# Kernel tuning notes

Measured on AMD Instinct MI355X. Metric: run time of the kernel, lower is better.

## Reference

```python
import jax, jax.numpy as jnp
import numpy as np

B = 8192          # batch of sequences (original module used 1; math broadcasts)
T = 99            # sequential FastGRNN steps
D_IN = 32         # per-step input features (3168 = 99 * 32)
D_H = 100         # hidden size
R_W, R_U = 16, 25 # low ranks
N_CLS = 6


def setup_inputs() -> dict:
    key = jax.random.key(0)
    ks = jax.random.split(key, 11)
    s = 0.1
    return {
        "x": jax.random.normal(ks[0], (B, T * D_IN), dtype=jnp.float32),
        "W1": jax.random.normal(ks[1], (D_IN, R_W), dtype=jnp.float32) * s,
        "W2": jax.random.normal(ks[2], (R_W, D_H), dtype=jnp.float32) * s,
        "U1": jax.random.normal(ks[3], (D_H, R_U), dtype=jnp.float32) * s,
        "U2": jax.random.normal(ks[4], (R_U, D_H), dtype=jnp.float32) * s,
        "bias_gate": jax.random.normal(ks[5], (1, D_H), dtype=jnp.float32) * s,
        "bias_update": jax.random.normal(ks[6], (1, D_H), dtype=jnp.float32) * s,
        "zeta": jax.random.normal(ks[7], (1, 1), dtype=jnp.float32),
        "nu": jax.random.normal(ks[8], (1, 1), dtype=jnp.float32),
        "FC": jax.random.normal(ks[9], (D_H, N_CLS), dtype=jnp.float32) * s,
        "FCbias": jax.random.normal(ks[10], (1, N_CLS), dtype=jnp.float32) * s,
    }


def reference(x, W1, W2, U1, U2, bias_gate, bias_update, zeta, nu, FC, FCbias):
    b = x.shape[0]
    # x[:, 32*i:32*(i+1)] for i in 0..T-1  ->  [T, B, D_IN] for scan
    xs = x.reshape(b, T, D_IN).transpose(1, 0, 2)
    sz = jax.nn.sigmoid(zeta)  # [1,1]
    sn = jax.nn.sigmoid(nu)    # [1,1]
    H0 = jnp.zeros((b, D_H), dtype=x.dtype)

    def step(H, XX):
        # low-rank projections: (XX @ W1) @ W2 + (H @ U1) @ U2
        c = (XX @ W1) @ W2 + (H @ U1) @ U2          # [B, D_H]
        g = jax.nn.sigmoid(c + bias_gate)
        h = jnp.tanh(c + bias_update)
        # exact blend from source: tanh branch is NOT scaled by (1-g)
        H_new = g * H + (sz * (1.0 - g) + sn * h)
        return H_new, None

    H, _ = jax.lax.scan(step, H0, xs)
    score = H @ FC + FCbias                          # [B, N_CLS]
    return score
```

## Files before the change

kernel.cpp:

```cpp
#include <hip/hip_runtime.h>
#include <math.h>


typedef __attribute__((ext_vector_type(8))) short short8_t;
typedef __attribute__((ext_vector_type(4))) float f32x4;

#define TSTEPS 99
#define DIN    32
#define DH     100
#define XROW   3168
#define NCLS   6
#define LOG2E  1.44269504088896340736f

#define NFRAG  70
#define OFF_EG (NFRAG * 256)
#define OFF_EU (OFF_EG + 128)
#define OFF_SZ (OFF_EU + 128)
#define OFF_SN (OFF_SZ + 1)

__device__ __forceinline__ unsigned cvtpk(float a, float b) {
    unsigned r;
    asm("v_cvt_pk_bf16_f32 %0, %1, %2" : "=v"(r) : "v"(a), "v"(b));
    return r;
}
__device__ __forceinline__ float fbits(unsigned u) { return __int_as_float((int)u); }

union F8 { unsigned u4[4]; short8_t s8; };

__global__ __launch_bounds__(256) void precomp(
    const float* __restrict__ W1, const float* __restrict__ W2,
    const float* __restrict__ U1, const float* __restrict__ U2,
    const float* __restrict__ bg, const float* __restrict__ bu,
    const float* __restrict__ zeta, const float* __restrict__ nu,
    float* __restrict__ ws)
{
    const int i = blockIdx.x * 256 + threadIdx.x;
    if (i < 2240) {
        const int lane = i & 63, f = i >> 6;
        const int jt = f / 5, kt = f % 5;
        const int u = lane & 15, g4 = lane >> 4;
        const int col = jt * 16 + u;
        float v[8];
        #pragma unroll
        for (int e = 0; e < 8; ++e) {
            float s = 0.f;
            if (col < DH) {
                if (kt < 4) {
                    const int k = kt * 32 + g4 * 8 + e;
                    if (k < DH) {
                        #pragma unroll
                        for (int r = 0; r < 25; ++r)
                            s = fmaf(U1[k * 25 + r], U2[r * DH + col], s);
                    }
                } else {
                    const int k = g4 * 8 + e;
                    #pragma unroll
                    for (int r = 0; r < 16; ++r)
                        s = fmaf(W1[k * 16 + r], W2[r * DH + col], s);
                }
            }
            v[e] = s * LOG2E;
        }
        unsigned hi[4], lo[4];
        #pragma unroll
        for (int rr = 0; rr < 4; ++rr) {
            const float a = v[2 * rr], b = v[2 * rr + 1];
            const unsigned ph = cvtpk(a, b);
            hi[rr] = ph;
            lo[rr] = cvtpk(a - fbits(ph << 16), b - fbits(ph & 0xffff0000u));
        }
        uint4* B = (uint4*)ws;
        B[(f * 2 + 0) * 64 + lane] = make_uint4(hi[0], hi[1], hi[2], hi[3]);
        B[(f * 2 + 1) * 64 + lane] = make_uint4(lo[0], lo[1], lo[2], lo[3]);
    } else if (i < 2240 + 128) {
        const int p = i - 2240;
        ws[OFF_EG + p] = (p < DH) ? expf(-bg[p]) : 1.f;
    } else if (i < 2240 + 256) {
        const int p = i - 2240 - 128;
        ws[OFF_EU + p] = (p < DH) ? expf(-2.f * bu[p]) : 1.f;
    } else if (i == 2240 + 256) {
        ws[OFF_SZ] = 1.f / (1.f + expf(-zeta[0]));
    } else if (i == 2240 + 257) {
        ws[OFF_SN] = 1.f / (1.f + expf(-nu[0]));
    }
}

__global__ __launch_bounds__(256, 2) void fastgrnn_main(
    const float* __restrict__ x, const float* __restrict__ ws,
    const float* __restrict__ FC, const float* __restrict__ FCbias,
    float* __restrict__ out)
{
    __shared__ __align__(16) float Hl[2][16][132];

    const int tid  = threadIdx.x;
    const int lane = tid & 63;
    const int ww   = __builtin_amdgcn_readfirstlane(tid >> 6);
    const int jn   = (ww == 3) ? 1 : 2;
    const int u    = lane & 15;
    const int g4   = lane >> 4;
    const int rowbase = blockIdx.x * 16;

    for (int z = tid; z < 2 * 16 * 132; z += 256) ((float*)Hl)[z] = 0.f;

    F8 Breg[2][5][2];
    #pragma unroll
    for (int jj = 0; jj < 2; ++jj) {
        const int jt = (2 * ww + jj > 6) ? 6 : 2 * ww + jj;
        #pragma unroll
        for (int kt = 0; kt < 5; ++kt) {
            #pragma unroll
            for (int s = 0; s < 2; ++s) {
                const int F = (jt * 5 + kt) * 2 + s;
                Breg[jj][kt][s].s8 =
                    *(const short8_t*)((const uint4*)ws + F * 64 + lane);
                asm volatile("" : "+v"(Breg[jj][kt][s].u4[0]),
                                  "+v"(Breg[jj][kt][s].u4[1]),
                                  "+v"(Breg[jj][kt][s].u4[2]),
                                  "+v"(Breg[jj][kt][s].u4[3]));
            }
        }
    }
    float eg_r[2], eu_r[2];
    #pragma unroll
    for (int jj = 0; jj < 2; ++jj) {
        const int jt = (2 * ww + jj > 6) ? 6 : 2 * ww + jj;
        const int unit = jt * 16 + u;
        eg_r[jj] = ws[OFF_EG + unit];
        eu_r[jj] = ws[OFF_EU + unit];
        asm volatile("" : "+v"(eg_r[jj]), "+v"(eu_r[jj]));
    }
    const float sz = ws[OFF_SZ];
    const float sn = ws[OFF_SN];

    const float* __restrict__ xrow = x + (size_t)(rowbase + u) * XROW + g4 * 8;

    const f32x4 zero4 = {0.f, 0.f, 0.f, 0.f};
    f32x4 Hold[2];
    Hold[0] = zero4; Hold[1] = zero4;

    __syncthreads();

    for (int t = 0; t < TSTEPS; ++t) {
        const int rb = t & 1, wb = rb ^ 1;

        F8 xhi, xlo;
        {
            const f32x4 xa = *(const f32x4*)(xrow + t * DIN);
            const f32x4 xb = *(const f32x4*)(xrow + t * DIN + 4);
            const float xs[8] = { xa.x, xa.y, xa.z, xa.w, xb.x, xb.y, xb.z, xb.w };
            #pragma unroll
            for (int r = 0; r < 4; ++r) {
                const unsigned ph = cvtpk(xs[2*r], xs[2*r+1]);
                xhi.u4[r] = ph;
                xlo.u4[r] = cvtpk(xs[2*r]   - fbits(ph << 16),
                                  xs[2*r+1] - fbits(ph & 0xffff0000u));
            }
        }

        F8 ahi[4], alo[4];
        #pragma unroll
        for (int kt = 0; kt < 4; ++kt) {
            const f32x4 h0 = *(const f32x4*)&Hl[rb][u][kt * 32 + g4 * 8];
            const f32x4 h1 = *(const f32x4*)&Hl[rb][u][kt * 32 + g4 * 8 + 4];
            const float hs[8] = { h0.x, h0.y, h0.z, h0.w, h1.x, h1.y, h1.z, h1.w };
            #pragma unroll
            for (int r = 0; r < 4; ++r) {
                const unsigned ph = cvtpk(hs[2*r], hs[2*r+1]);
                ahi[kt].u4[r] = ph;
                alo[kt].u4[r] = cvtpk(hs[2*r]   - fbits(ph << 16),
                                      hs[2*r+1] - fbits(ph & 0xffff0000u));
            }
        }

        f32x4 acc[2];
        acc[0] = zero4; acc[1] = zero4;

        #pragma unroll
        for (int kt = 0; kt < 5; ++kt) {
            const short8_t Ah = (kt < 4) ? ahi[kt].s8 : xhi.s8;
            const short8_t Al = (kt < 4) ? alo[kt].s8 : xlo.s8;
            #pragma unroll
            for (int jj = 0; jj < 2; ++jj)
                if (jj < jn)
                    acc[jj] = __builtin_amdgcn_mfma_f32_16x16x32_bf16(
                        Al, Breg[jj][kt][0].s8, acc[jj], 0, 0, 0);
            #pragma unroll
            for (int jj = 0; jj < 2; ++jj)
                if (jj < jn)
                    acc[jj] = __builtin_amdgcn_mfma_f32_16x16x32_bf16(
                        Ah, Breg[jj][kt][1].s8, acc[jj], 0, 0, 0);
            #pragma unroll
            for (int jj = 0; jj < 2; ++jj)
                if (jj < jn)
                    acc[jj] = __builtin_amdgcn_mfma_f32_16x16x32_bf16(
                        Ah, Breg[jj][kt][0].s8, acc[jj], 0, 0, 0);
        }

        #pragma unroll
        for (int jj = 0; jj < 2; ++jj) {
            if (jj < jn) {
                f32x4 hn;
                #pragma unroll
                for (int i = 0; i < 4; ++i) {
                    const float cc = acc[jj][i];
                    const float E  = __builtin_amdgcn_exp2f(-cc);
                    const float g  = __builtin_amdgcn_rcpf(fmaf(E, eg_r[jj], 1.f));
                    float p = E * E * eu_r[jj];
                    p = fminf(p, 1e30f);
                    const float h = (1.f - p) * __builtin_amdgcn_rcpf(1.f + p);
                    hn[i] = fmaf(g, Hold[jj][i], fmaf(sn, h, fmaf(-sz, g, sz)));
                }
                Hold[jj] = hn;
                const int unit = (2 * ww + jj) * 16 + u;
                Hl[wb][g4 * 4 + 0][unit] = hn[0];
                Hl[wb][g4 * 4 + 1][unit] = hn[1];
                Hl[wb][g4 * 4 + 2][unit] = hn[2];
                Hl[wb][g4 * 4 + 3][unit] = hn[3];
            }
        }
        __syncthreads();
    }

    const int fb = TSTEPS & 1;
    if (tid < 16 * NCLS) {
        const int rl = tid / NCLS, c = tid % NCLS;
        float s = FCbias[c];
        for (int k = 0; k < DH; ++k)
            s = fmaf(Hl[fb][rl][k], FC[k * NCLS + c], s);
        out[(size_t)(rowbase + rl) * NCLS + c] = s;
    }
}

extern "C" void kernel_launch(void* const* d_in, const int* in_sizes, int n_in,
                              void* d_out, int out_size, void* d_ws, size_t ws_size,
                              hipStream_t stream)
{
    const float* x    = (const float*)d_in[0];
    const float* W1   = (const float*)d_in[1];
    const float* W2   = (const float*)d_in[2];
    const float* U1   = (const float*)d_in[3];
    const float* U2   = (const float*)d_in[4];
    const float* bg   = (const float*)d_in[5];
    const float* bu   = (const float*)d_in[6];
    const float* zeta = (const float*)d_in[7];
    const float* nu   = (const float*)d_in[8];
    const float* FC   = (const float*)d_in[9];
    const float* FCb  = (const float*)d_in[10];
    float* ws  = (float*)d_ws;
    float* out = (float*)d_out;

    precomp<<<(2240 + 258 + 255) / 256, 256, 0, stream>>>(
        W1, W2, U1, U2, bg, bu, zeta, nu, ws);
    fastgrnn_main<<<512, 256, 0, stream>>>(x, ws, FC, FCb, out);
}
```

Before: 311.1 us.

## Store hidden state as pre-split bf16 hi/lo pairs in swizzled LDS

```diff
diff --git a/kernel.cpp b/kernel.cpp
--- a/kernel.cpp
+++ b/kernel.cpp
@@ -90,7 +90,7 @@
     const float* __restrict__ FC, const float* __restrict__ FCbias,
     float* __restrict__ out)
 {
-    __shared__ __align__(16) float Hl[2][16][132];
+    __shared__ unsigned Hs[2][2][16][68];
 
     const int tid  = threadIdx.x;
     const int lane = tid & 63;
@@ -100,7 +100,7 @@
     const int g4   = lane >> 4;
     const int rowbase = blockIdx.x * 16;
 
-    for (int z = tid; z < 2 * 16 * 132; z += 256) ((float*)Hl)[z] = 0.f;
+    for (int z = tid; z < 2 * 2 * 16 * 68; z += 256) ((unsigned*)Hs)[z] = 0u;
 
     F8 Breg[2][5][2];
     #pragma unroll
@@ -138,6 +138,9 @@
     f32x4 Hold[2];
     Hold[0] = zero4; Hold[1] = zero4;
 
+    const int ridx0 = (g4 ^ (u & 3)) << 2;
+    unsigned short* const hwbase = (unsigned short*)&Hs[0][0][0][0];
+
     __syncthreads();
 
     for (int t = 0; t < TSTEPS; ++t) {
@@ -157,28 +160,14 @@
             }
         }
 
-        F8 ahi[4], alo[4];
+        f32x4 a0[2], a1[2];
+        a0[0] = zero4; a0[1] = zero4; a1[0] = zero4; a1[1] = zero4;
+
         #pragma unroll
         for (int kt = 0; kt < 4; ++kt) {
-            const f32x4 h0 = *(const f32x4*)&Hl[rb][u][kt * 32 + g4 * 8];
-            const f32x4 h1 = *(const f32x4*)&Hl[rb][u][kt * 32 + g4 * 8 + 4];
-            const float hs[8] = { h0.x, h0.y, h0.z, h0.w, h1.x, h1.y, h1.z, h1.w };
-            #pragma unroll
-            for (int r = 0; r < 4; ++r) {
-                const unsigned ph = cvtpk(hs[2*r], hs[2*r+1]);
-                ahi[kt].u4[r] = ph;
-                alo[kt].u4[r] = cvtpk(hs[2*r]   - fbits(ph << 16),
-                                      hs[2*r+1] - fbits(ph & 0xffff0000u));
-            }
-        }
-
-        f32x4 acc[2];
-        acc[0] = zero4; acc[1] = zero4;
-
-        #pragma unroll
-        for (int kt = 0; kt < 5; ++kt) {
-            const short8_t Ah = (kt < 4) ? ahi[kt].s8 : xhi.s8;
-            const short8_t Al = (kt < 4) ? alo[kt].s8 : xlo.s8;
+            const short8_t Ah = *(const short8_t*)&Hs[rb][0][u][kt * 16 + ridx0];
+            const short8_t Al = *(const short8_t*)&Hs[rb][1][u][kt * 16 + ridx0];
+            f32x4* acc = (kt & 1) ? a1 : a0;
             #pragma unroll
             for (int jj = 0; jj < 2; ++jj)
                 if (jj < jn)
@@ -195,27 +184,52 @@
                     acc[jj] = __builtin_amdgcn_mfma_f32_16x16x32_bf16(
                         Ah, Breg[jj][kt][0].s8, acc[jj], 0, 0, 0);
         }
-
+        #pragma unroll
+        for (int jj = 0; jj < 2; ++jj)
+            if (jj < jn)
+                a1[jj] = __builtin_amdgcn_mfma_f32_16x16x32_bf16(
+                    xlo.s8, Breg[jj][4][0].s8, a1[jj], 0, 0, 0);
+        #pragma unroll
+        for (int jj = 0; jj < 2; ++jj)
+            if (jj < jn)
+                a1[jj] = __builtin_amdgcn_mfma_f32_16x16x32_bf16(
+                    xhi.s8, Breg[jj][4][1].s8, a1[jj], 0, 0, 0);
+        #pragma unroll
+        for (int jj = 0; jj < 2; ++jj)
+            if (jj < jn)
+                a1[jj] = __builtin_amdgcn_mfma_f32_16x16x32_bf16(
+                    xhi.s8, Breg[jj][4][0].s8, a1[jj], 0, 0, 0);
+
+        unsigned short* const hp = hwbase + wb * (2 * 16 * 136);
+        unsigned short* const lp = hp + 16 * 136;
         #pragma unroll
         for (int jj = 0; jj < 2; ++jj) {
             if (jj < jn) {
+                const int jt = (2 * ww + jj > 6) ? 6 : 2 * ww + jj;
+                const int pbase = jt * 8 + (u >> 1);
+                const int hoff  = (u & 1);
                 f32x4 hn;
                 #pragma unroll
                 for (int i = 0; i < 4; ++i) {
-                    const float cc = acc[jj][i];
+                    const float cc = a0[jj][i] + a1[jj][i];
                     const float E  = __builtin_amdgcn_exp2f(-cc);
                     const float g  = __builtin_amdgcn_rcpf(fmaf(E, eg_r[jj], 1.f));
-                    float p = E * E * eu_r[jj];
-                    p = fminf(p, 1e30f);
-                    const float h = (1.f - p) * __builtin_amdgcn_rcpf(1.f + p);
+                    const float pp = fmaf(E * E, eu_r[jj], 1.f);
+                    const float h  = fmaf(2.f, __builtin_amdgcn_rcpf(pp), -1.f);
                     hn[i] = fmaf(g, Hold[jj][i], fmaf(sn, h, fmaf(-sz, g, sz)));
                 }
                 Hold[jj] = hn;
-                const int unit = (2 * ww + jj) * 16 + u;
-                Hl[wb][g4 * 4 + 0][unit] = hn[0];
-                Hl[wb][g4 * 4 + 1][unit] = hn[1];
-                Hl[wb][g4 * 4 + 2][unit] = hn[2];
-                Hl[wb][g4 * 4 + 3][unit] = hn[3];
+                #pragma unroll
+                for (int i = 0; i < 4; ++i) {
+                    const int r  = g4 * 4 + i;
+                    const int ps = pbase ^ (i << 2);
+                    const float h = hn[i];
+                    const unsigned h16 = cvtpk(h, h);
+                    const float    hrec = fbits(h16 << 16);
+                    const unsigned l16 = cvtpk(h - hrec, h - hrec);
+                    hp[r * 136 + ps * 2 + hoff] = (unsigned short)h16;
+                    lp[r * 136 + ps * 2 + hoff] = (unsigned short)l16;
+                }
             }
         }
         __syncthreads();
@@ -225,8 +239,15 @@
     if (tid < 16 * NCLS) {
         const int rl = tid / NCLS, c = tid % NCLS;
         float s = FCbias[c];
-        for (int k = 0; k < DH; ++k)
-            s = fmaf(Hl[fb][rl][k], FC[k * NCLS + c], s);
+        for (int k = 0; k < DH; ++k) {
+            const int p  = k >> 1;
+            const int ps = p ^ ((rl & 3) << 2);
+            const unsigned wh = Hs[fb][0][rl][ps];
+            const unsigned wl = Hs[fb][1][rl][ps];
+            const float hi = (k & 1) ? fbits(wh & 0xffff0000u) : fbits(wh << 16);
+            const float lo = (k & 1) ? fbits(wl & 0xffff0000u) : fbits(wl << 16);
+            s = fmaf(hi + lo, FC[k * NCLS + c], s);
+        }
         out[(size_t)(rowbase + rl) * NCLS + c] = s;
     }
 }
```

After: 319.1 us. 2.6% more time.
